# Optimization experiments

Measured on AMD Instinct MI355X. Metric: run time of the kernel, lower is better.

## Reference

```python
import jax, jax.numpy as jnp
import numpy as np

M, D, HID = 4096, 100, 256  # paths, state dim, hidden width (fixed at 256 in neural_net)


def setup_inputs() -> dict:
    key = jax.random.key(0)
    k1, k2, k3, k4, k5, k6 = jax.random.split(key, 6)
    t = jax.random.uniform(k1, (M, 1), dtype=jnp.float32)            # times in [0, T=1]
    X = jax.random.uniform(k2, (M, D), dtype=jnp.float32) + 0.5      # positive asset prices
    fan_in, fan_out = D + 1, HID
    lim = float(np.sqrt(6.0 / (fan_in + fan_out)))                   # xavier_uniform (torch init)
    W1 = jax.random.uniform(k3, (HID, D + 1), minval=-lim, maxval=lim, dtype=jnp.float32)
    bl = float(1.0 / np.sqrt(D + 1))
    b1 = jax.random.uniform(k4, (HID,), minval=-bl, maxval=bl, dtype=jnp.float32)
    ol = float(1.0 / np.sqrt(HID))
    W2 = jax.random.uniform(k5, (1, HID), minval=-ol, maxval=ol, dtype=jnp.float32)
    b2 = jax.random.uniform(k6, (1,), minval=-ol, maxval=ol, dtype=jnp.float32)
    return {"t": t, "X": X, "W1": W1, "b1": b1, "W2": W2, "b2": b2}


def reference(t, X, W1, b1, W2, b2):
    """Faithful JAX version of FBSNN.net_u_Du: u, du/dx, du/dt and the
    per-sample Hessian w.r.t. x of u = out(sin(fc_1([t, x])))."""
    inputs = jnp.concatenate([t, X], axis=1)  # (M, D+1)

    def f_scalar(s):  # s: (D+1,) -> scalar u
        return (jnp.sin(s @ W1.T + b1) @ W2.T + b2)[0]

    u = jax.vmap(f_scalar)(inputs)[:, None]               # (M, 1)
    g = jax.vmap(jax.grad(f_scalar))(inputs)              # (M, D+1)
    DuDt = g[:, :1]                                       # (M, 1)
    DuDx = g[:, 1:]                                       # (M, D)
    Hfull = jax.vmap(jax.hessian(f_scalar))(inputs)       # (M, D+1, D+1), batched (no Python loop)
    D2uDx2 = Hfull[:, 1:, 1:]                             # (M, D, D) == hessian[1:, 1:] per sample
    return (u, DuDx, DuDt, D2uDx2)
```

## Files before the change

kernel.cpp:

```cpp
#include <hip/hip_runtime.h>
#include <hip/hip_bf16.h>

#define M_SAMP 4096
#define D_IN   100
#define HID    256
#define IN_DIM 101
#define NSQ    10000
#define NPAD   10112
#define SMF    4
#define NFWD   (M_SAMP / SMF)

typedef __attribute__((ext_vector_type(8))) short short8;
typedef __attribute__((ext_vector_type(4))) float f32x4;

__device__ __forceinline__ void gload_lds16(const void* g, void* l) {
    __builtin_amdgcn_global_load_lds(
        (const __attribute__((address_space(1))) void*)g,
        (__attribute__((address_space(3))) void*)l, 16, 0, 0);
}

__global__ __launch_bounds__(256) void k_pre(
        const float* __restrict__ t, const float* __restrict__ X,
        const float* __restrict__ W1, const float* __restrict__ b1,
        const float* __restrict__ W2, const float* __restrict__ b2,
        float* __restrict__ u_out, float* __restrict__ dux,
        float* __restrict__ dut, __hip_bfloat16* __restrict__ S2n,
        __hip_bfloat16* __restrict__ P) {
    __shared__ __align__(16) char smem[51200];
    int tid = threadIdx.x, bid = blockIdx.x;

    if (bid < NFWD) {
        float* s_in  = (float*)smem;
        float* c_sh  = (float*)(smem + 1664);
        float* us_sh = (float*)(smem + 1664 + 4096);
        int i0 = bid * SMF;

        for (int idx = tid; idx < SMF * IN_DIM; idx += 256) {
            int i = idx / IN_DIM, j = idx % IN_DIM;
            s_in[i * IN_DIM + j] = (j == 0) ? t[i0 + i]
                                            : X[(size_t)(i0 + i) * D_IN + (j - 1)];
        }
        __syncthreads();

        int h = tid;
        float z[SMF];
        float bb = b1[h];
#pragma unroll
        for (int i = 0; i < SMF; i++) z[i] = bb;
        const float* wrow = W1 + (size_t)h * IN_DIM;
        for (int j = 0; j < IN_DIM; j++) {
            float w = wrow[j];
#pragma unroll
            for (int i = 0; i < SMF; i++) z[i] += w * s_in[i * IN_DIM + j];
        }
        float w2 = W2[h];
#pragma unroll
        for (int i = 0; i < SMF; i++) {
            float sz, cz;
            sincosf(z[i], &sz, &cz);
            c_sh[i * HID + h]  = w2 * cz;
            us_sh[i * HID + h] = w2 * sz;
            S2n[(size_t)(i0 + i) * HID + h] = __float2bfloat16(-w2 * sz);
        }
        __syncthreads();

        for (int off = 128; off > 0; off >>= 1) {
            if (tid < off) {
#pragma unroll
                for (int i = 0; i < SMF; i++)
                    us_sh[i * HID + tid] += us_sh[i * HID + tid + off];
            }
            __syncthreads();
        }
        if (tid < SMF) u_out[i0 + tid] = us_sh[tid * HID] + b2[0];

        if (tid < IN_DIM) {
            float acc[SMF];
#pragma unroll
            for (int i = 0; i < SMF; i++) acc[i] = 0.f;
            for (int h0 = 0; h0 < HID; h0 += 4) {
                float w0 = W1[(size_t)(h0 + 0) * IN_DIM + tid];
                float w1 = W1[(size_t)(h0 + 1) * IN_DIM + tid];
                float w2_ = W1[(size_t)(h0 + 2) * IN_DIM + tid];
                float w3 = W1[(size_t)(h0 + 3) * IN_DIM + tid];
#pragma unroll
                for (int i = 0; i < SMF; i++)
                    acc[i] += c_sh[i * HID + h0] * w0 + c_sh[i * HID + h0 + 1] * w1
                            + c_sh[i * HID + h0 + 2] * w2_ + c_sh[i * HID + h0 + 3] * w3;
            }
            if (tid == 0) {
                for (int i = 0; i < SMF; i++) dut[i0 + i] = acc[i];
            } else {
                for (int i = 0; i < SMF; i++)
                    dux[(size_t)(i0 + i) * D_IN + (tid - 1)] = acc[i];
            }
        }
    } else if (bid < NFWD + D_IN) {
        int j = bid - NFWD;
        __hip_bfloat16* Wb = (__hip_bfloat16*)smem;
        const float* wrow = W1 + (size_t)tid * IN_DIM + 1;
        for (int k = 0; k < D_IN; k++)
            Wb[k * HID + tid] = __float2bfloat16(wrow[k]);
        __syncthreads();

        int ksub = tid >> 5, h8 = (tid & 31) * 8;
        float aj[8];
#pragma unroll
        for (int e = 0; e < 8; e++) aj[e] = __bfloat162float(Wb[j * HID + h8 + e]);

        for (int kk = 0; kk < 104; kk += 8) {
            int k = kk + ksub;
            if (k < D_IN) {
                short8 v;
#pragma unroll
                for (int e = 0; e < 8; e++) {
                    float b = __bfloat162float(Wb[k * HID + h8 + e]);
                    __hip_bfloat16 hv = __float2bfloat16(aj[e] * b);
                    v[e] = *reinterpret_cast<short*>(&hv);
                }
                *(short8*)&P[(size_t)(j * D_IN + k) * HID + h8] = v;
            }
        }
    } else {
        short8 zero = {0, 0, 0, 0, 0, 0, 0, 0};
        size_t base = (size_t)NSQ * HID;
        for (int idx = tid; idx < (NPAD - NSQ) * HID / 8; idx += 256)
            *(short8*)&P[base + (size_t)idx * 8] = zero;
    }
}

#define BM 128
#define BN 128
#define BK 64
#define NK 4
#define NBLK 79

__global__ __launch_bounds__(256) void k_gemm(
        const __hip_bfloat16* __restrict__ A,
        const __hip_bfloat16* __restrict__ B,
        float* __restrict__ C) {
    __shared__ __hip_bfloat16 As[2][BM * BK];
    __shared__ __hip_bfloat16 Bs[2][BM * BK];

    int bid = blockIdx.x;
    int xcd = bid & 7, i = bid >> 3;
    int bn = i >> 2;
    int bm = xcd * 4 + (i & 3);
    int m0 = bm * BM, n0 = bn * BN;
    int tid = threadIdx.x;
    int lane = tid & 63, wave = tid >> 6;
    int wm = wave >> 1, wn = wave & 1;

    int srow8 = lane >> 3;
    int scol = ((lane & 7) ^ srow8) * 8;

    f32x4 acc[4][4];
#pragma unroll
    for (int ii = 0; ii < 4; ii++)
#pragma unroll
        for (int j = 0; j < 4; j++) acc[ii][j] = {0.f, 0.f, 0.f, 0.f};

    auto stage = [&](int buf, int kt) {
        int kc = kt * BK;
#pragma unroll
        for (int q = 0; q < 4; q++) {
            int rb = wave * 32 + q * 8;
            gload_lds16(A + (size_t)(m0 + rb + srow8) * HID + kc + scol,
                        &As[buf][rb * BK]);
            gload_lds16(B + (size_t)(n0 + rb + srow8) * HID + kc + scol,
                        &Bs[buf][rb * BK]);
        }
    };

    stage(0, 0);

    for (int kt = 0; kt < NK; kt++) {
        int cur = kt & 1;
        __syncthreads();
        if (kt + 1 < NK) stage(cur ^ 1, kt + 1);

        const char* Ab = (const char*)As[cur];
        const char* Bb = (const char*)Bs[cur];
        int lo = lane & 15;
        int xr = (lane & 7) << 4;
#pragma unroll
        for (int kk = 0; kk < 2; kk++) {
            int kbs = (kk * 64 + ((lane >> 4) << 4)) ^ xr;
            short8 af[4], bf4[4];
#pragma unroll
            for (int mi = 0; mi < 4; mi++)
                af[mi] = *(const short8*)(Ab + (wm * 64 + mi * 16 + lo) * 128 + kbs);
#pragma unroll
            for (int ni = 0; ni < 4; ni++)
                bf4[ni] = *(const short8*)(Bb + (wn * 64 + ni * 16 + lo) * 128 + kbs);
#pragma unroll
            for (int mi = 0; mi < 4; mi++)
#pragma unroll
                for (int ni = 0; ni < 4; ni++)
                    acc[mi][ni] = __builtin_amdgcn_mfma_f32_16x16x32_bf16(
                        bf4[ni], af[mi], acc[mi][ni], 0, 0, 0);
        }
    }

    int lo = lane & 15, hi4 = (lane >> 4) << 2;
#pragma unroll
    for (int mi = 0; mi < 4; mi++) {
        int mrow = m0 + wm * 64 + mi * 16 + lo;
#pragma unroll
        for (int ni = 0; ni < 4; ni++) {
            int ncol = n0 + wn * 64 + ni * 16 + hi4;
            if (ncol < NSQ)
                *(f32x4*)&C[(size_t)mrow * NSQ + ncol] = acc[mi][ni];
        }
    }
}

extern "C" void kernel_launch(void* const* d_in, const int* in_sizes, int n_in,
                              void* d_out, int out_size, void* d_ws, size_t ws_size,
                              hipStream_t stream) {
    const float* t  = (const float*)d_in[0];
    const float* X  = (const float*)d_in[1];
    const float* W1 = (const float*)d_in[2];
    const float* b1 = (const float*)d_in[3];
    const float* W2 = (const float*)d_in[4];
    const float* b2 = (const float*)d_in[5];

    float* out = (float*)d_out;
    float* u_out = out;
    float* dux   = out + M_SAMP;
    float* dut   = out + M_SAMP + (size_t)M_SAMP * D_IN;
    float* H     = dut + M_SAMP;

    char* ws = (char*)d_ws;
    __hip_bfloat16* S2n = (__hip_bfloat16*)ws;
    __hip_bfloat16* P   = (__hip_bfloat16*)(ws + 2097152);

    k_pre<<<NFWD + D_IN + 1, 256, 0, stream>>>(t, X, W1, b1, W2, b2,
                                               u_out, dux, dut, S2n, P);
    k_gemm<<<(M_SAMP / BM) * NBLK, 256, 0, stream>>>(S2n, P, H);
}
```

Before: 86.18 us.

## Transpose W1 once, widen forward batching, split gradient reduction, spread P build

A small new kernel writes a transposed copy of W1 to workspace and zero-fills the padded rows of P. The forward pass then reads W1T coalesced, handles 8 samples per block instead of 4, and splits the gradient dot product across both 128-thread halves with an LDS reduction. The pairwise-product matrix P is now built by 632 blocks of 16 rows each, straight from W1T, instead of 100 blocks that each staged all of W1 in LDS. This adds a launch and intermediate traffic but aims to remove strided global loads and the load imbalance of the P-building blocks.

```diff
diff --git a/kernel.cpp b/kernel.cpp
--- a/kernel.cpp
+++ b/kernel.cpp
@@ -7,8 +7,9 @@
 #define IN_DIM 101
 #define NSQ    10000
 #define NPAD   10112
-#define SMF    4
+#define SMF    8
 #define NFWD   (M_SAMP / SMF)
+#define NPG    632
 
 typedef __attribute__((ext_vector_type(8))) short short8;
 typedef __attribute__((ext_vector_type(4))) float f32x4;
@@ -19,20 +20,35 @@
         (__attribute__((address_space(3))) void*)l, 16, 0, 0);
 }
 
-__global__ __launch_bounds__(256) void k_pre(
+__global__ __launch_bounds__(256) void k_w1t(const float* __restrict__ W1,
+                                             float* __restrict__ W1T,
+                                             __hip_bfloat16* __restrict__ P) {
+    int bid = blockIdx.x, tid = threadIdx.x;
+    if (bid < IN_DIM) {
+        W1T[bid * HID + tid] = W1[tid * IN_DIM + bid];
+    } else {
+        short8 zero = {0, 0, 0, 0, 0, 0, 0, 0};
+        size_t base = (size_t)NSQ * HID;
+        for (int idx = tid; idx < (NPAD - NSQ) * HID / 8; idx += 256)
+            *(short8*)&P[base + (size_t)idx * 8] = zero;
+    }
+}
+
+__global__ __launch_bounds__(256) void k_mid(
         const float* __restrict__ t, const float* __restrict__ X,
-        const float* __restrict__ W1, const float* __restrict__ b1,
+        const float* __restrict__ W1T, const float* __restrict__ b1,
         const float* __restrict__ W2, const float* __restrict__ b2,
         float* __restrict__ u_out, float* __restrict__ dux,
         float* __restrict__ dut, __hip_bfloat16* __restrict__ S2n,
         __hip_bfloat16* __restrict__ P) {
-    __shared__ __align__(16) char smem[51200];
+    __shared__ __align__(16) char smem[23296];
     int tid = threadIdx.x, bid = blockIdx.x;
 
     if (bid < NFWD) {
         float* s_in  = (float*)smem;
-        float* c_sh  = (float*)(smem + 1664);
-        float* us_sh = (float*)(smem + 1664 + 4096);
+        float* c_sh  = (float*)(smem + 3264);
+        float* us_sh = (float*)(smem + 3264 + 8192);
+        float* g_sh  = (float*)(smem + 3264 + 16384);
         int i0 = bid * SMF;
 
         for (int idx = tid; idx < SMF * IN_DIM; idx += 256) {
@@ -47,9 +63,8 @@
         float bb = b1[h];
 #pragma unroll
         for (int i = 0; i < SMF; i++) z[i] = bb;
-        const float* wrow = W1 + (size_t)h * IN_DIM;
         for (int j = 0; j < IN_DIM; j++) {
-            float w = wrow[j];
+            float w = W1T[j * HID + h];
 #pragma unroll
             for (int i = 0; i < SMF; i++) z[i] += w * s_in[i * IN_DIM + j];
         }
@@ -74,58 +89,67 @@
         }
         if (tid < SMF) u_out[i0 + tid] = us_sh[tid * HID] + b2[0];
 
-        if (tid < IN_DIM) {
-            float acc[SMF];
-#pragma unroll
-            for (int i = 0; i < SMF; i++) acc[i] = 0.f;
-            for (int h0 = 0; h0 < HID; h0 += 4) {
-                float w0 = W1[(size_t)(h0 + 0) * IN_DIM + tid];
-                float w1 = W1[(size_t)(h0 + 1) * IN_DIM + tid];
-                float w2_ = W1[(size_t)(h0 + 2) * IN_DIM + tid];
-                float w3 = W1[(size_t)(h0 + 3) * IN_DIM + tid];
+        int j = tid & 127, grp = tid >> 7;
+        bool act = (j < IN_DIM);
+        float acc[SMF];
+#pragma unroll
+        for (int i = 0; i < SMF; i++) acc[i] = 0.f;
+        if (act) {
+            int hbase = grp * 128;
+            for (int h0 = 0; h0 < 128; h0 += 4) {
+                float w0 = W1T[(size_t)j * HID + hbase + h0];
+                float w1 = W1T[(size_t)j * HID + hbase + h0 + 1];
+                float w2_ = W1T[(size_t)j * HID + hbase + h0 + 2];
+                float w3 = W1T[(size_t)j * HID + hbase + h0 + 3];
 #pragma unroll
                 for (int i = 0; i < SMF; i++)
-                    acc[i] += c_sh[i * HID + h0] * w0 + c_sh[i * HID + h0 + 1] * w1
-                            + c_sh[i * HID + h0 + 2] * w2_ + c_sh[i * HID + h0 + 3] * w3;
-            }
-            if (tid == 0) {
+                    acc[i] += c_sh[i * HID + hbase + h0] * w0
+                            + c_sh[i * HID + hbase + h0 + 1] * w1
+                            + c_sh[i * HID + hbase + h0 + 2] * w2_
+                            + c_sh[i * HID + hbase + h0 + 3] * w3;
+            }
+        }
+        if (grp == 1 && act) {
+#pragma unroll
+            for (int i = 0; i < SMF; i++) g_sh[i * IN_DIM + j] = acc[i];
+        }
+        __syncthreads();
+        if (grp == 0 && act) {
+#pragma unroll
+            for (int i = 0; i < SMF; i++) acc[i] += g_sh[i * IN_DIM + j];
+            if (j == 0) {
                 for (int i = 0; i < SMF; i++) dut[i0 + i] = acc[i];
             } else {
                 for (int i = 0; i < SMF; i++)
-                    dux[(size_t)(i0 + i) * D_IN + (tid - 1)] = acc[i];
-            }
-        }
-    } else if (bid < NFWD + D_IN) {
-        int j = bid - NFWD;
-        __hip_bfloat16* Wb = (__hip_bfloat16*)smem;
-        const float* wrow = W1 + (size_t)tid * IN_DIM + 1;
-        for (int k = 0; k < D_IN; k++)
-            Wb[k * HID + tid] = __float2bfloat16(wrow[k]);
-        __syncthreads();
-
+                    dux[(size_t)(i0 + i) * D_IN + (j - 1)] = acc[i];
+            }
+        }
+    } else {
+        int n0p = (bid - NFWD) * 16;
         int ksub = tid >> 5, h8 = (tid & 31) * 8;
-        float aj[8];
-#pragma unroll
-        for (int e = 0; e < 8; e++) aj[e] = __bfloat162float(Wb[j * HID + h8 + e]);
-
-        for (int kk = 0; kk < 104; kk += 8) {
-            int k = kk + ksub;
-            if (k < D_IN) {
+#pragma unroll
+        for (int p = 0; p < 2; p++) {
+            int n = n0p + ksub + p * 8;
+            if (n < NSQ) {
+                int j = n / D_IN, k = n - j * D_IN;
+                const float* wj = &W1T[(size_t)(1 + j) * HID + h8];
+                const float* wk = &W1T[(size_t)(1 + k) * HID + h8];
+                f32x4 aj0 = *(const f32x4*)wj, aj1 = *(const f32x4*)(wj + 4);
+                f32x4 bk0 = *(const f32x4*)wk, bk1 = *(const f32x4*)(wk + 4);
                 short8 v;
 #pragma unroll
-                for (int e = 0; e < 8; e++) {
-                    float b = __bfloat162float(Wb[k * HID + h8 + e]);
-                    __hip_bfloat16 hv = __float2bfloat16(aj[e] * b);
+                for (int e = 0; e < 4; e++) {
+                    __hip_bfloat16 hv = __float2bfloat16(aj0[e] * bk0[e]);
                     v[e] = *reinterpret_cast<short*>(&hv);
                 }
-                *(short8*)&P[(size_t)(j * D_IN + k) * HID + h8] = v;
-            }
-        }
-    } else {
-        short8 zero = {0, 0, 0, 0, 0, 0, 0, 0};
-        size_t base = (size_t)NSQ * HID;
-        for (int idx = tid; idx < (NPAD - NSQ) * HID / 8; idx += 256)
-            *(short8*)&P[base + (size_t)idx * 8] = zero;
+#pragma unroll
+                for (int e = 0; e < 4; e++) {
+                    __hip_bfloat16 hv = __float2bfloat16(aj1[e] * bk1[e]);
+                    v[4 + e] = *reinterpret_cast<short*>(&hv);
+                }
+                *(short8*)&P[(size_t)n * HID + h8] = v;
+            }
+        }
     }
 }
 
@@ -234,8 +258,10 @@
     char* ws = (char*)d_ws;
     __hip_bfloat16* S2n = (__hip_bfloat16*)ws;
     __hip_bfloat16* P   = (__hip_bfloat16*)(ws + 2097152);
-
-    k_pre<<<NFWD + D_IN + 1, 256, 0, stream>>>(t, X, W1, b1, W2, b2,
-                                               u_out, dux, dut, S2n, P);
+    float* W1T          = (float*)(ws + 2097152 + 5242880);
+
+    k_w1t<<<IN_DIM + 1, 256, 0, stream>>>(W1, W1T, P);
+    k_mid<<<NFWD + NPG, 256, 0, stream>>>(t, X, W1T, b1, W2, b2,
+                                          u_out, dux, dut, S2n, P);
     k_gemm<<<(M_SAMP / BM) * NBLK, 256, 0, stream>>>(S2n, P, H);
 }
```

After: 76.57 us. -11.1%, faster.
